# Performance work log

Measured on AMD Instinct MI355X. Metric: run time of the kernel, lower is better.

## Reference

```python
import jax, jax.numpy as jnp
import numpy as np
import math

B, L, D = 4, 4096, 768          # batch, seq_len (== l_max), d_model
ORDER, EMB_DIM = 16, 3          # hyena_filter_order, hyena_emb_dim
W_MOD = 1.0                     # hyena_w_mod
FAST, SLOW, TARGET = 0.3, 1.5, 1e-2  # ExponentialModulation defaults


def setup_inputs() -> dict:
    key = jax.random.key(0)
    ks = jax.random.split(key, 16)
    n = lambda i, shape, s: jax.random.normal(ks[i], shape, dtype=jnp.float32) * s
    # PositionalEmbedding buffer/param z, deterministic Hyena init (seq_len = l_max = L)
    t = np.linspace(0.0, 1.0, L)[None, :, None]
    bands = (EMB_DIM - 1) // 2
    t_re = np.linspace(0, L - 1, L)[None, :, None]
    w = 2 * math.pi * t_re / L
    f = np.linspace(1e-4, bands - 1, bands)[None, None]
    zc = np.exp(-1j * f * w)
    z = np.concatenate([t, zc.real, zc.imag], axis=-1).astype(np.float32)  # (1, L, 3)
    return {
        "u": jax.random.normal(ks[0], (B, L, D), dtype=jnp.float32),
        "w_in": n(1, (3 * D, D), 0.02),
        "b_in": jnp.zeros((3 * D,), jnp.float32),
        "w_out": n(2, (D, D), 0.02),
        "b_out": jnp.zeros((D,), jnp.float32),
        "conv_w": n(3, (3 * D, 1, 3), 0.3),   # depthwise Conv1d weight (O, I/groups=1, K)
        "conv_b": jnp.zeros((3 * D,), jnp.float32),
        "z": jnp.asarray(z),
        "fw1": n(4, (ORDER, EMB_DIM), 0.3),
        "fb1": n(5, (ORDER,), 0.3),
        "fw2": n(6, (ORDER, ORDER), 0.3),
        "fb2": n(7, (ORDER,), 0.3),
        "fw3": n(8, (ORDER, ORDER), 0.3),
        "fb3": n(9, (ORDER,), 0.3),
        "fw4": n(10, (D, ORDER), 0.3),
        "freq": jnp.full((1, ORDER), 10.0, jnp.float32),  # shared Sin freq, init w*ones
        "filter_bias": jax.random.normal(ks[11], (D,), dtype=jnp.float32),
    }


def _hyena_filter(z, fw1, fb1, fw2, fb2, fw3, fb3, fw4, freq, Lq):
    # implicit MLP with SHARED Sin activation (same freq param at all 3 activations)
    sin = lambda h: jnp.sin(W_MOD * freq * h)
    h = sin(z @ fw1.T + fb1)
    h = sin(h @ fw2.T + fb2)
    h = sin(h @ fw3.T + fb3)
    h = h @ fw4.T                                     # (1, L, D)
    # ExponentialModulation
    max_d = math.log(TARGET) / FAST
    min_d = math.log(TARGET) / SLOW
    deltas = jnp.linspace(min_d, max_d, D)[None, None]  # (1, 1, D)
    t = jnp.linspace(0.0, 1.0, Lq)[None, :, None]       # (1, L, 1)
    h = h * jnp.exp(-t * jnp.abs(deltas))
    return h[0].T                                      # (D, L)


def _fftconv(v, k, bias):
    # causal FFT long conv: fft_size = 2L, torch norm='forward' conventions
    Lq = v.shape[-1]
    nfft = 2 * Lq
    k_f = jnp.fft.rfft(k, n=nfft) / nfft               # (D, nfft//2+1)
    v_f = jnp.fft.rfft(v, n=nfft)                      # (B, D, nfft//2+1)
    y = jnp.fft.irfft(v_f * k_f, n=nfft, norm="forward")[..., :Lq]
    return y + v * bias[None, :, None]


def reference(u, w_in, b_in, w_out, b_out, conv_w, conv_b, z,
              fw1, fb1, fw2, fb2, fw3, fb3, fw4, freq, filter_bias):
    Bq, Lq, Dq = u.shape
    x = u @ w_in.T + b_in                              # (B, L, 3D)
    x = x.transpose(0, 2, 1)                           # (B, 3D, L)
    # depthwise short conv, kernel 3, padding 2, sliced to [:L]
    xc = jax.lax.conv_general_dilated(
        x, conv_w, window_strides=(1,), padding=[(2, 2)],
        feature_group_count=3 * Dq,
        dimension_numbers=("NCH", "OIH", "NCH"))[..., :Lq]
    xc = xc + conv_b[None, :, None]
    x1, x2, v = jnp.split(xc, 3, axis=1)               # each (B, D, L)
    v = v * x1                                         # pre-gate
    k = _hyena_filter(z[:, :Lq], fw1, fb1, fw2, fb2, fw3, fb3, fw4, freq, Lq)
    y = _fftconv(v, k, filter_bias) * x2               # long conv + post-gate
    y = y.transpose(0, 2, 1) @ w_out.T + b_out         # (B, L, D)
    return y
```

## Files before the change

kernel.cpp:

```cpp
#include <hip/hip_runtime.h>

#define BB 4
#define LL 4096
#define DD 768
#define TD 2304
#define NFFT 8192
#define PI2 6.283185307179586f

__device__ __forceinline__ unsigned short f2b(float f) {
    unsigned u = __float_as_uint(f);
    unsigned r = (u + 0x7fffu + ((u >> 16) & 1u)) >> 16;
    return (unsigned short)r;
}
__device__ __forceinline__ float b2f(unsigned short h) {
    return __uint_as_float((unsigned)h << 16);
}
__device__ __forceinline__ unsigned cvt_pk_bf16(float lo, float hi) {
    unsigned r;
    asm("v_cvt_pk_bf16_f32 %0, %1, %2" : "=v"(r) : "v"(lo), "v"(hi));
    return r;
}

typedef __bf16 bf16x8 __attribute__((ext_vector_type(8)));
typedef float  f32x4  __attribute__((ext_vector_type(4)));

constexpr float TWC[16] = {
    1.f, 0.98078528f, 0.92387953f, 0.83146961f,
    0.70710678f, 0.55557023f, 0.38268343f, 0.19509032f,
    0.f, -0.19509032f, -0.38268343f, -0.55557023f,
    -0.70710678f, -0.83146961f, -0.92387953f, -0.98078528f};
constexpr float TWS[16] = {
    0.f, 0.19509032f, 0.38268343f, 0.55557023f,
    0.70710678f, 0.83146961f, 0.92387953f, 0.98078528f,
    1.f, 0.98078528f, 0.92387953f, 0.83146961f,
    0.70710678f, 0.55557023f, 0.38268343f, 0.19509032f};

template<int LOGN, bool INV>
__device__ __forceinline__ void reg_fft(float2* R) {
    constexpr int N = 1 << LOGN;
#pragma unroll
    for (int i = 0; i < N; ++i) {
        int j = 0;
#pragma unroll
        for (int b = 0; b < LOGN; ++b) if (i & (1 << b)) j |= (1 << (LOGN - 1 - b));
        if (j > i) { float2 tt = R[i]; R[i] = R[j]; R[j] = tt; }
    }
#pragma unroll
    for (int s = 1; s <= LOGN; ++s) {
        const int hm = 1 << (s - 1);
        const int tsh = 5 - s;
#pragma unroll
        for (int g = 0; g < N; g += (hm << 1)) {
#pragma unroll
            for (int j2 = 0; j2 < hm; ++j2) {
                const float wr = TWC[j2 << tsh];
                const float wi = INV ? TWS[j2 << tsh] : -TWS[j2 << tsh];
                float2 u = R[g + j2];
                float2 v = R[g + j2 + hm];
                float vr = v.x * wr - v.y * wi;
                float vi = v.x * wi + v.y * wr;
                R[g + j2]      = make_float2(u.x + vr, u.y + vi);
                R[g + j2 + hm] = make_float2(u.x - vr, u.y - vi);
            }
        }
    }
}

template<int NN>
__device__ __forceinline__ void ramp_mul(float2* R, float ang) {
    float s0, c0; __sincosf(ang, &s0, &c0);
    float wr = c0, wi = s0;
#pragma unroll
    for (int k = 1; k < NN; ++k) {
        float xr = R[k].x, xi = R[k].y;
        R[k] = make_float2(xr * wr - xi * wi, xr * wi + xi * wr);
        float nr = wr * c0 - wi * s0;
        float ni = wr * s0 + wi * c0;
        wr = nr; wi = ni;
    }
}

#define A1(t, k2) ((k2) * 288 + (t) + ((t) >> 3))
#define A2(k2, p, r) ((k2) * 272 + (r) * 17 + (p))
#define FFT_LDS 9216

__device__ __forceinline__ void eng_fwd(float2* buf, float2* R, int t) {
    reg_fft<5, false>(R);
    ramp_mul<32>(R, -PI2 * (float)t / 8192.0f);
    __syncthreads();
#pragma unroll
    for (int k2 = 0; k2 < 32; ++k2) buf[A1(t, k2)] = R[k2];
    __syncthreads();
    const int p = t & 15, c2 = (t >> 4) << 1;
#pragma unroll
    for (int q = 0; q < 16; ++q) {
        R[q]      = buf[A1(p + 16 * q, c2)];
        R[16 + q] = buf[A1(p + 16 * q, c2 + 1)];
    }
    reg_fft<4, false>(R);
    reg_fft<4, false>(R + 16);
    float a2 = -PI2 * (float)p / 256.0f;
    ramp_mul<16>(R, a2);
    ramp_mul<16>(R + 16, a2);
    __syncthreads();
#pragma unroll
    for (int r = 0; r < 16; ++r) {
        buf[A2(c2, p, r)]     = R[r];
        buf[A2(c2 + 1, p, r)] = R[16 + r];
    }
    __syncthreads();
    const int rr = p;
#pragma unroll
    for (int pp = 0; pp < 16; ++pp) {
        R[pp]      = buf[A2(c2, pp, rr)];
        R[16 + pp] = buf[A2(c2 + 1, pp, rr)];
    }
    reg_fft<4, false>(R);
    reg_fft<4, false>(R + 16);
}

__device__ __forceinline__ void eng_inv(float2* buf, float2* R, int t) {
    const int p = t & 15, c2 = (t >> 4) << 1, rr = p;
    reg_fft<4, true>(R);
    reg_fft<4, true>(R + 16);
    __syncthreads();
#pragma unroll
    for (int pp = 0; pp < 16; ++pp) {
        buf[A2(c2, pp, rr)]     = R[pp];
        buf[A2(c2 + 1, pp, rr)] = R[16 + pp];
    }
    __syncthreads();
#pragma unroll
    for (int r = 0; r < 16; ++r) {
        R[r]      = buf[A2(c2, p, r)];
        R[16 + r] = buf[A2(c2 + 1, p, r)];
    }
    float a2 = PI2 * (float)p / 256.0f;
    ramp_mul<16>(R, a2);
    ramp_mul<16>(R + 16, a2);
    reg_fft<4, true>(R);
    reg_fft<4, true>(R + 16);
    __syncthreads();
#pragma unroll
    for (int q = 0; q < 16; ++q) {
        buf[A1(p + 16 * q, c2)]     = R[q];
        buf[A1(p + 16 * q, c2 + 1)] = R[16 + q];
    }
    __syncthreads();
#pragma unroll
    for (int k2 = 0; k2 < 32; ++k2) R[k2] = buf[A1(t, k2)];
    ramp_mul<32>(R, PI2 * (float)t / 8192.0f);
    reg_fft<5, true>(R);
}

__global__ __launch_bounds__(256) void k_cast_pair(
        const float* __restrict__ srcA, unsigned long long nA4,
        const float* __restrict__ srcB, unsigned long long nB4,
        unsigned short* __restrict__ dstA, unsigned short* __restrict__ dstB) {
    unsigned long long i = (unsigned long long)blockIdx.x * 256 + threadIdx.x;
    const float* s; unsigned short* d;
    if (i < nA4)            { s = srcA + i * 4;         d = dstA + i * 4; }
    else if (i < nA4 + nB4) { unsigned long long j = i - nA4; s = srcB + j * 4; d = dstB + j * 4; }
    else return;
    float4 v = *(const float4*)s;
    unsigned long long p = (unsigned long long)f2b(v.x)
                         | ((unsigned long long)f2b(v.y) << 16)
                         | ((unsigned long long)f2b(v.z) << 32)
                         | ((unsigned long long)f2b(v.w) << 48);
    *(unsigned long long*)d = p;
}

#define GEMM_CORE                                                               \
    __shared__ unsigned char AsB[16384];                                        \
    __shared__ unsigned char BsB[16384];                                        \
    const int tid  = threadIdx.x;                                               \
    const int lane = tid & 63;                                                  \
    const int w    = tid >> 6;                                                  \
    const int wr   = w >> 1, wc = w & 1;                                        \
    const int nbx  = (int)gridDim.x;                                            \
    int bid = (int)blockIdx.y * nbx + (int)blockIdx.x;                          \
    { const int cpx = (nbx * (int)gridDim.y) >> 3;                              \
      bid = (bid & 7) * cpx + (bid >> 3); }                                     \
    const int m0 = (bid / nbx) * 128, n0 = (bid % nbx) * 128;                   \
    f32x4 acc[4][4] = {};                                                       \
    const int srow = lane >> 3;                    \
    const int sslot = (lane & 7) ^ srow;          \
    for (int k0 = 0; k0 < K; k0 += 64) {                                        \
        _Pragma("unroll")                                                       \
        for (int c = 0; c < 4; ++c) {                                           \
            int chunk = w * 4 + c;                                              \
            int row = chunk * 8 + srow;                                         \
            const char* ga = (const char*)A  + (((size_t)(m0 + row) * K + k0) * 2) + sslot * 16; \
            __builtin_amdgcn_global_load_lds(                                   \
                (const __attribute__((address_space(1))) void*)ga,              \
                (__attribute__((address_space(3))) void*)(AsB + chunk * 1024), 16, 0, 0); \
            const char* gb = (const char*)Bw + (((size_t)(n0 + row) * K + k0) * 2) + sslot * 16; \
            __builtin_amdgcn_global_load_lds(                                   \
                (const __attribute__((address_space(1))) void*)gb,              \
                (__attribute__((address_space(3))) void*)(BsB + chunk * 1024), 16, 0, 0); \
        }                                                                       \
        __syncthreads();                                                        \
        const int quad = lane >> 4;                                             \
        const int rsel = lane & 15;                                             \
        _Pragma("unroll")                                                       \
        for (int kk = 0; kk < 2; ++kk) {                                        \
            bf16x8 af[4], bfr[4];                                               \
            _Pragma("unroll")                                                   \
            for (int i = 0; i < 4; ++i) {                                       \
                int rowA = wr * 64 + i * 16 + rsel;                             \
                int slotA = (kk * 4 + quad) ^ (rsel & 7);                       \
                af[i]  = *(const bf16x8*)(AsB + rowA * 128 + slotA * 16);       \
                int rowB = wc * 64 + i * 16 + rsel;                             \
                bfr[i] = *(const bf16x8*)(BsB + rowB * 128 + slotA * 16);       \
            }                                                                   \
            _Pragma("unroll")                                                   \
            for (int i = 0; i < 4; ++i)                                         \
                _Pragma("unroll")                                               \
                for (int j = 0; j < 4; ++j)                                     \
                    acc[i][j] = __builtin_amdgcn_mfma_f32_16x16x32_bf16(af[i], bfr[j], acc[i][j], 0, 0, 0); \
        }                                                                       \
        __syncthreads();                                                        \
    }

__global__ __launch_bounds__(256) void k_gemm1_xt(
        const unsigned short* __restrict__ A, const unsigned short* __restrict__ Bw,
        const float* __restrict__ bias, unsigned short* __restrict__ xT,
        int K) {
    GEMM_CORE
    const int cq = lane >> 4;
    const int cn = lane & 15;
    const int b  = m0 >> 12;
    const int lb = (m0 & 4095) + wr * 64 + cq * 4;
#pragma unroll
    for (int j = 0; j < 4; ++j) {
        int col = n0 + wc * 64 + j * 16 + cn;
        float bv = bias[col];
        unsigned short* cp = xT + ((size_t)b * TD + col) * LL + lb;
#pragma unroll
        for (int i = 0; i < 4; ++i) {
            uint2 p;
            p.x = cvt_pk_bf16(acc[i][j][0] + bv, acc[i][j][1] + bv);
            p.y = cvt_pk_bf16(acc[i][j][2] + bv, acc[i][j][3] + bv);
            *(uint2*)(cp + i * 16) = p;
        }
    }
}

__global__ __launch_bounds__(256) void k_gemm_mfma(
        const unsigned short* __restrict__ A, const unsigned short* __restrict__ Bw,
        const float* __restrict__ bias, float* __restrict__ C,
        int N, int K) {
    GEMM_CORE
    const int cq = lane >> 4;
    const int cn = lane & 15;
#pragma unroll
    for (int j = 0; j < 4; ++j) {
        int col = n0 + wc * 64 + j * 16 + cn;
        float bv = bias[col];
#pragma unroll
        for (int i = 0; i < 4; ++i) {
            int rbase = m0 + wr * 64 + i * 16 + cq * 4;
#pragma unroll
            for (int r = 0; r < 4; ++r)
                C[(size_t)(rbase + r) * N + col] = acc[i][j][r] + bv;
        }
    }
}

__device__ __forceinline__ void ld_row18(const unsigned short* __restrict__ r,
                                         int l0, float* a) {
    unsigned ql = 0;
    if (l0 >= 2) ql = *(const unsigned*)(r + l0 - 2);
    a[0] = b2f((unsigned short)(ql & 0xffffu));
    a[1] = b2f((unsigned short)(ql >> 16));
    uint4 q0 = *(const uint4*)(r + l0);
    uint4 q1 = *(const uint4*)(r + l0 + 8);
    unsigned qq[8] = {q0.x, q0.y, q0.z, q0.w, q1.x, q1.y, q1.z, q1.w};
#pragma unroll
    for (int k2 = 0; k2 < 8; ++k2) {
        a[2 + 2 * k2] = b2f((unsigned short)(qq[k2] & 0xffffu));
        a[3 + 2 * k2] = b2f((unsigned short)(qq[k2] >> 16));
    }
}

__global__ __launch_bounds__(256) void k_shortconv_t(
        const unsigned short* __restrict__ xT,
        const float* __restrict__ conv_w, const float* __restrict__ conv_b,
        unsigned short* __restrict__ vbuf, unsigned short* __restrict__ x2buf) {
    const int bd = blockIdx.x;
    const int b  = bd / DD;
    const int d  = bd - b * DD;
    const int l0 = (int)threadIdx.x << 4;
    const unsigned short* r1 = xT + ((size_t)b * TD + d) * LL;
    const unsigned short* r2 = r1 + (size_t)DD * LL;
    const unsigned short* r3 = r2 + (size_t)DD * LL;
    const float w10 = conv_w[3*d],          w11 = conv_w[3*d+1],          w12 = conv_w[3*d+2];
    const float w20 = conv_w[3*(DD+d)],     w21 = conv_w[3*(DD+d)+1],     w22 = conv_w[3*(DD+d)+2];
    const float w30 = conv_w[3*(2*DD+d)],   w31 = conv_w[3*(2*DD+d)+1],   w32 = conv_w[3*(2*DD+d)+2];
    const float c1 = conv_b[d], c2 = conv_b[DD + d], c3 = conv_b[2*DD + d];
    float a1[18], a2[18], a3[18];
    ld_row18(r1, l0, a1);
    ld_row18(r2, l0, a2);
    ld_row18(r3, l0, a3);
    unsigned pv[8], px[8];
#pragma unroll
    for (int k2 = 0; k2 < 8; ++k2) {
        float x1a = w10*a1[2*k2]   + w11*a1[2*k2+1] + w12*a1[2*k2+2] + c1;
        float x1b = w10*a1[2*k2+1] + w11*a1[2*k2+2] + w12*a1[2*k2+3] + c1;
        float x2a = w20*a2[2*k2]   + w21*a2[2*k2+1] + w22*a2[2*k2+2] + c2;
        float x2b = w20*a2[2*k2+1] + w21*a2[2*k2+2] + w22*a2[2*k2+3] + c2;
        float va  = w30*a3[2*k2]   + w31*a3[2*k2+1] + w32*a3[2*k2+2] + c3;
        float vb  = w30*a3[2*k2+1] + w31*a3[2*k2+2] + w32*a3[2*k2+3] + c3;
        pv[k2] = cvt_pk_bf16(va * x1a, vb * x1b);
        px[k2] = cvt_pk_bf16(x2a, x2b);
    }
    unsigned short* ov = vbuf  + ((size_t)b * DD + d) * LL + l0;
    unsigned short* ox = x2buf + ((size_t)b * DD + d) * LL + l0;
    *(uint4*)(ov)     = make_uint4(pv[0], pv[1], pv[2], pv[3]);
    *(uint4*)(ov + 8) = make_uint4(pv[4], pv[5], pv[6], pv[7]);
    *(uint4*)(ox)     = make_uint4(px[0], px[1], px[2], px[3]);
    *(uint4*)(ox + 8) = make_uint4(px[4], px[5], px[6], px[7]);
}

__global__ __launch_bounds__(256) void k_filter_mlp(
        const float* __restrict__ z,
        const float* __restrict__ fw1, const float* __restrict__ fb1,
        const float* __restrict__ fw2, const float* __restrict__ fb2,
        const float* __restrict__ fw3, const float* __restrict__ fb3,
        const float* __restrict__ freq, float* __restrict__ h3g) {
    int l = blockIdx.x * 256 + threadIdx.x;
    float z0 = z[l*3+0], z1 = z[l*3+1], z2 = z[l*3+2];
    float h1[16], h2[16];
#pragma unroll
    for (int j = 0; j < 16; ++j) {
        float a = z0*fw1[j*3+0] + z1*fw1[j*3+1] + z2*fw1[j*3+2] + fb1[j];
        h1[j] = sinf(freq[j] * a);
    }
#pragma unroll
    for (int j = 0; j < 16; ++j) {
        float a = fb2[j];
#pragma unroll
        for (int i = 0; i < 16; ++i) a += h1[i] * fw2[j*16+i];
        h2[j] = sinf(freq[j] * a);
    }
#pragma unroll
    for (int j = 0; j < 16; ++j) {
        float a = fb3[j];
#pragma unroll
        for (int i = 0; i < 16; ++i) a += h2[i] * fw3[j*16+i];
        h3g[j * LL + l] = sinf(freq[j] * a);
    }
}

__global__ __launch_bounds__(256) void k_filter_fft(
        const float* __restrict__ h3g, const float* __restrict__ fw4,
        const float* __restrict__ fbias, float2* __restrict__ kf) {
    __shared__ float2 buf[FFT_LDS];
    const int d = blockIdx.x, t = threadIdx.x;
    float w4[16];
#pragma unroll
    for (int i = 0; i < 16; ++i) w4[i] = fw4[d * 16 + i];
    const float min_d = 3.070113457325394f;
    const float max_d = 15.35056728662697f;
    const float ad = min_d + (max_d - min_d) * ((float)d / 767.0f);
    float2 R[32];
#pragma unroll
    for (int j = 0; j < 16; ++j) {
        int l = t + 256 * j;
        float acc = 0.f;
#pragma unroll
        for (int i = 0; i < 16; ++i) acc += h3g[i * LL + l] * w4[i];
        acc *= __expf(-((float)l / 4095.0f) * ad);
        R[j] = make_float2(acc, 0.f);
        R[16 + j] = make_float2(0.f, 0.f);
    }
    eng_fwd(buf, R, t);
    const float fb = fbias[d];
    const float inv_n = 1.0f / (float)NFFT;
    float2* kd = kf + (size_t)d * NFFT;
#pragma unroll
    for (int i = 0; i < 32; ++i)
        kd[i * 256 + t] = make_float2((R[i].x + fb) * inv_n, R[i].y * inv_n);
}

__global__ __launch_bounds__(256) void k_fftconv3(
        const unsigned short* __restrict__ vbuf, const float2* __restrict__ kf,
        unsigned short* __restrict__ x2y) {
    __shared__ float2 buf[FFT_LDS];
    const int bp = blockIdx.x;
    const int d = bp % DD;
    const int bpair = bp / DD;
    const size_t row1 = (size_t)(bpair * 2) * DD + d;
    const size_t row2 = row1 + DD;
    const unsigned short* v1 = vbuf + row1 * LL;
    const unsigned short* v2 = vbuf + row2 * LL;
    const int t = threadIdx.x;
    float2 R[32];
#pragma unroll
    for (int j = 0; j < 16; ++j) {
        int idx = t + 256 * j;
        R[j] = make_float2(b2f(v1[idx]), b2f(v2[idx]));
        R[16 + j] = make_float2(0.f, 0.f);
    }
    eng_fwd(buf, R, t);
    const float2* kd = kf + (size_t)d * NFFT;
#pragma unroll
    for (int i = 0; i < 32; ++i) {
        float2 w = kd[i * 256 + t];
        float2 zv = R[i];
        R[i] = make_float2(zv.x * w.x - zv.y * w.y, zv.x * w.y + zv.y * w.x);
    }
    eng_inv(buf, R, t);
    unsigned short* o1 = x2y + row1 * LL;
    unsigned short* o2 = x2y + row2 * LL;
#pragma unroll
    for (int j = 0; j < 16; ++j) {
        int idx = t + 256 * j;
        o1[idx] = f2b(R[j].x * b2f(o1[idx]));
        o2[idx] = f2b(R[j].y * b2f(o2[idx]));
    }
}

__global__ __launch_bounds__(256) void k_transpose_cast(
        const unsigned short* __restrict__ yg, unsigned short* __restrict__ ygT) {
    __shared__ float t[64][65];
    const int b = blockIdx.z;
    const int d0 = blockIdx.y * 64;
    const int l0 = blockIdx.x * 64;
    for (int idx = threadIdx.x; idx < 4096; idx += 256) {
        int r = idx >> 6, c = idx & 63;
        t[r][c] = b2f(yg[((size_t)(b * DD + d0 + r)) * LL + l0 + c]);
    }
    __syncthreads();
    for (int idx = threadIdx.x; idx < 2048; idx += 256) {
        int r = idx >> 5, c = (idx & 31) * 2;
        unsigned int p = (unsigned int)f2b(t[c][r]) | ((unsigned int)f2b(t[c+1][r]) << 16);
        *(unsigned int*)&ygT[((size_t)(b * LL + l0 + r)) * DD + d0 + c] = p;
    }
}

extern "C" void kernel_launch(void* const* d_in, const int* in_sizes, int n_in,
                              void* d_out, int out_size, void* d_ws, size_t ws_size,
                              hipStream_t stream) {
    const float* u      = (const float*)d_in[0];
    const float* w_in   = (const float*)d_in[1];
    const float* b_in   = (const float*)d_in[2];
    const float* w_out  = (const float*)d_in[3];
    const float* b_out  = (const float*)d_in[4];
    const float* conv_w = (const float*)d_in[5];
    const float* conv_b = (const float*)d_in[6];
    const float* z      = (const float*)d_in[7];
    const float* fw1    = (const float*)d_in[8];
    const float* fb1    = (const float*)d_in[9];
    const float* fw2    = (const float*)d_in[10];
    const float* fb2    = (const float*)d_in[11];
    const float* fw3    = (const float*)d_in[12];
    const float* fb3    = (const float*)d_in[13];
    const float* fw4    = (const float*)d_in[14];
    const float* freq   = (const float*)d_in[15];
    const float* fbias  = (const float*)d_in[16];

    char* ws = (char*)d_ws;
    unsigned short* x_bf     = (unsigned short*)(ws);
    float2* kf               = (float2*)(ws);
    float*  h3g              = (float*)(ws + 50331648);
    unsigned short* w_out_bf = (unsigned short*)(ws + 50593792);
    unsigned short* ygT      = (unsigned short*)(ws + 63176704);
    unsigned short* vbuf     = (unsigned short*)(ws + 150994944);
    unsigned short* x2y      = (unsigned short*)(ws + 176160768);
    unsigned short* u_bf     = (unsigned short*)(ws + 201326592);
    unsigned short* w_in_bf  = (unsigned short*)(ws + 226492416);

    k_cast_pair<<<(3145728 + 442368 + 255) / 256, 256, 0, stream>>>(
        u, 3145728ULL, w_in, 442368ULL, u_bf, w_in_bf);
    k_gemm1_xt<<<dim3(TD/128, (BB*LL)/128), 256, 0, stream>>>(u_bf, w_in_bf, b_in, x_bf, DD);
    k_shortconv_t<<<BB*DD, 256, 0, stream>>>(x_bf, conv_w, conv_b, vbuf, x2y);
    k_filter_mlp<<<LL/256, 256, 0, stream>>>(z, fw1, fb1, fw2, fb2, fw3, fb3, freq, h3g);
    k_filter_fft<<<DD, 256, 0, stream>>>(h3g, fw4, fbias, kf);
    k_cast_pair<<<(147456 + 255) / 256, 256, 0, stream>>>(
        w_out, 147456ULL, (const float*)0, 0ULL, w_out_bf, (unsigned short*)0);
    k_fftconv3<<<(BB/2)*DD, 256, 0, stream>>>(vbuf, kf, x2y);
    k_transpose_cast<<<dim3(LL/64, DD/64, BB), 256, 0, stream>>>(x2y, ygT);
    k_gemm_mfma<<<dim3(DD/128, (BB*LL)/128), 256, 0, stream>>>(ygT, w_out_bf, b_out, (float*)d_out, DD, DD);
}
```

Measured before the change: 410.3 us.

## Fuse depthwise short conv into FFT long-conv kernel, one block per channel

Folds the short convolution and pre-gate into the FFT convolution kernel. The conv output now goes through LDS into the FFT registers instead of being written as bf16 v and x2 buffers and read back. Each block handles one channel across all four batches (two batch pairs), so the filter spectrum is loaded once and reused. This removes a kernel launch and a global round trip of intermediates, but cuts the grid to 768 blocks, which lowers parallelism and occupancy. The workspace is laid out again so kf no longer aliases the GEMM output.

```diff
diff --git a/kernel.cpp b/kernel.cpp
--- a/kernel.cpp
+++ b/kernel.cpp
@@ -283,43 +283,82 @@
     }
 }
 
-__global__ __launch_bounds__(256) void k_shortconv_t(
+__global__ __launch_bounds__(256) void k_convfft(
         const unsigned short* __restrict__ xT,
         const float* __restrict__ conv_w, const float* __restrict__ conv_b,
-        unsigned short* __restrict__ vbuf, unsigned short* __restrict__ x2buf) {
-    const int bd = blockIdx.x;
-    const int b  = bd / DD;
-    const int d  = bd - b * DD;
-    const int l0 = (int)threadIdx.x << 4;
-    const unsigned short* r1 = xT + ((size_t)b * TD + d) * LL;
-    const unsigned short* r2 = r1 + (size_t)DD * LL;
-    const unsigned short* r3 = r2 + (size_t)DD * LL;
+        const float2* __restrict__ kf,
+        unsigned short* __restrict__ yg) {
+    __shared__ float2 buf[FFT_LDS];
+    const int d = blockIdx.x;
+    const int t = threadIdx.x;
+    const int l0 = t << 4;
     const float w10 = conv_w[3*d],          w11 = conv_w[3*d+1],          w12 = conv_w[3*d+2];
     const float w20 = conv_w[3*(DD+d)],     w21 = conv_w[3*(DD+d)+1],     w22 = conv_w[3*(DD+d)+2];
     const float w30 = conv_w[3*(2*DD+d)],   w31 = conv_w[3*(2*DD+d)+1],   w32 = conv_w[3*(2*DD+d)+2];
     const float c1 = conv_b[d], c2 = conv_b[DD + d], c3 = conv_b[2*DD + d];
-    float a1[18], a2[18], a3[18];
-    ld_row18(r1, l0, a1);
-    ld_row18(r2, l0, a2);
-    ld_row18(r3, l0, a3);
-    unsigned pv[8], px[8];
-#pragma unroll
-    for (int k2 = 0; k2 < 8; ++k2) {
-        float x1a = w10*a1[2*k2]   + w11*a1[2*k2+1] + w12*a1[2*k2+2] + c1;
-        float x1b = w10*a1[2*k2+1] + w11*a1[2*k2+2] + w12*a1[2*k2+3] + c1;
-        float x2a = w20*a2[2*k2]   + w21*a2[2*k2+1] + w22*a2[2*k2+2] + c2;
-        float x2b = w20*a2[2*k2+1] + w21*a2[2*k2+2] + w22*a2[2*k2+3] + c2;
-        float va  = w30*a3[2*k2]   + w31*a3[2*k2+1] + w32*a3[2*k2+2] + c3;
-        float vb  = w30*a3[2*k2+1] + w31*a3[2*k2+2] + w32*a3[2*k2+3] + c3;
-        pv[k2] = cvt_pk_bf16(va * x1a, vb * x1b);
-        px[k2] = cvt_pk_bf16(x2a, x2b);
-    }
-    unsigned short* ov = vbuf  + ((size_t)b * DD + d) * LL + l0;
-    unsigned short* ox = x2buf + ((size_t)b * DD + d) * LL + l0;
-    *(uint4*)(ov)     = make_uint4(pv[0], pv[1], pv[2], pv[3]);
-    *(uint4*)(ov + 8) = make_uint4(pv[4], pv[5], pv[6], pv[7]);
-    *(uint4*)(ox)     = make_uint4(px[0], px[1], px[2], px[3]);
-    *(uint4*)(ox + 8) = make_uint4(px[4], px[5], px[6], px[7]);
+    const float2* kd = kf + (size_t)d * NFFT;
+    float2 w[32];
+    float2*   vstage = buf;
+    unsigned* xstage = (unsigned*)(buf + 4096);
+
+#pragma unroll 1
+    for (int pair = 0; pair < 2; ++pair) {
+        const int b0 = pair * 2, b1 = b0 + 1;
+        {
+            float a[18], q1[16], vv0[16], vv1[16];
+            ld_row18(xT + ((size_t)b0 * TD + d) * LL, l0, a);
+#pragma unroll
+            for (int k = 0; k < 16; ++k) q1[k] = w10*a[k] + w11*a[k+1] + w12*a[k+2] + c1;
+            ld_row18(xT + ((size_t)b0 * TD + 2*DD + d) * LL, l0, a);
+#pragma unroll
+            for (int k = 0; k < 16; ++k) vv0[k] = (w30*a[k] + w31*a[k+1] + w32*a[k+2] + c3) * q1[k];
+            ld_row18(xT + ((size_t)b1 * TD + d) * LL, l0, a);
+#pragma unroll
+            for (int k = 0; k < 16; ++k) q1[k] = w10*a[k] + w11*a[k+1] + w12*a[k+2] + c1;
+            ld_row18(xT + ((size_t)b1 * TD + 2*DD + d) * LL, l0, a);
+#pragma unroll
+            for (int k = 0; k < 16; ++k) vv1[k] = (w30*a[k] + w31*a[k+1] + w32*a[k+2] + c3) * q1[k];
+#pragma unroll
+            for (int k = 0; k < 16; ++k) vstage[l0 + k] = make_float2(vv0[k], vv1[k]);
+            ld_row18(xT + ((size_t)b0 * TD + DD + d) * LL, l0, a);
+#pragma unroll
+            for (int k = 0; k < 16; ++k) q1[k] = w20*a[k] + w21*a[k+1] + w22*a[k+2] + c2;
+            ld_row18(xT + ((size_t)b1 * TD + DD + d) * LL, l0, a);
+#pragma unroll
+            for (int k = 0; k < 16; ++k)
+                xstage[l0 + k] = cvt_pk_bf16(q1[k], w20*a[k] + w21*a[k+1] + w22*a[k+2] + c2);
+        }
+        __syncthreads();
+        float2 R[32];
+        unsigned x2p[16];
+#pragma unroll
+        for (int j = 0; j < 16; ++j) {
+            int idx = t + 256 * j;
+            R[j] = vstage[idx];
+            x2p[j] = xstage[idx];
+            R[16 + j] = make_float2(0.f, 0.f);
+        }
+        if (pair == 0) {
+#pragma unroll
+            for (int i = 0; i < 32; ++i) w[i] = kd[i * 256 + t];
+        }
+        eng_fwd(buf, R, t);
+#pragma unroll
+        for (int i = 0; i < 32; ++i) {
+            float2 zv = R[i];
+            R[i] = make_float2(zv.x * w[i].x - zv.y * w[i].y, zv.x * w[i].y + zv.y * w[i].x);
+        }
+        eng_inv(buf, R, t);
+        unsigned short* o1 = yg + ((size_t)b0 * DD + d) * LL;
+        unsigned short* o2 = o1 + (size_t)DD * LL;
+#pragma unroll
+        for (int j = 0; j < 16; ++j) {
+            int idx = t + 256 * j;
+            o1[idx] = f2b(R[j].x * b2f((unsigned short)(x2p[j] & 0xffffu)));
+            o2[idx] = f2b(R[j].y * b2f((unsigned short)(x2p[j] >> 16)));
+        }
+        if (pair == 0) __syncthreads();
+    }
 }
 
 __global__ __launch_bounds__(256) void k_filter_mlp(
@@ -381,44 +420,6 @@
 #pragma unroll
     for (int i = 0; i < 32; ++i)
         kd[i * 256 + t] = make_float2((R[i].x + fb) * inv_n, R[i].y * inv_n);
-}
-
-__global__ __launch_bounds__(256) void k_fftconv3(
-        const unsigned short* __restrict__ vbuf, const float2* __restrict__ kf,
-        unsigned short* __restrict__ x2y) {
-    __shared__ float2 buf[FFT_LDS];
-    const int bp = blockIdx.x;
-    const int d = bp % DD;
-    const int bpair = bp / DD;
-    const size_t row1 = (size_t)(bpair * 2) * DD + d;
-    const size_t row2 = row1 + DD;
-    const unsigned short* v1 = vbuf + row1 * LL;
-    const unsigned short* v2 = vbuf + row2 * LL;
-    const int t = threadIdx.x;
-    float2 R[32];
-#pragma unroll
-    for (int j = 0; j < 16; ++j) {
-        int idx = t + 256 * j;
-        R[j] = make_float2(b2f(v1[idx]), b2f(v2[idx]));
-        R[16 + j] = make_float2(0.f, 0.f);
-    }
-    eng_fwd(buf, R, t);
-    const float2* kd = kf + (size_t)d * NFFT;
-#pragma unroll
-    for (int i = 0; i < 32; ++i) {
-        float2 w = kd[i * 256 + t];
-        float2 zv = R[i];
-        R[i] = make_float2(zv.x * w.x - zv.y * w.y, zv.x * w.y + zv.y * w.x);
-    }
-    eng_inv(buf, R, t);
-    unsigned short* o1 = x2y + row1 * LL;
-    unsigned short* o2 = x2y + row2 * LL;
-#pragma unroll
-    for (int j = 0; j < 16; ++j) {
-        int idx = t + 256 * j;
-        o1[idx] = f2b(R[j].x * b2f(o1[idx]));
-        o2[idx] = f2b(R[j].y * b2f(o2[idx]));
-    }
 }
 
 __global__ __launch_bounds__(256) void k_transpose_cast(
@@ -461,25 +462,23 @@
     const float* fbias  = (const float*)d_in[16];
 
     char* ws = (char*)d_ws;
-    unsigned short* x_bf     = (unsigned short*)(ws);
-    float2* kf               = (float2*)(ws);
-    float*  h3g              = (float*)(ws + 50331648);
-    unsigned short* w_out_bf = (unsigned short*)(ws + 50593792);
-    unsigned short* ygT      = (unsigned short*)(ws + 63176704);
-    unsigned short* vbuf     = (unsigned short*)(ws + 150994944);
-    unsigned short* x2y      = (unsigned short*)(ws + 176160768);
-    unsigned short* u_bf     = (unsigned short*)(ws + 201326592);
-    unsigned short* w_in_bf  = (unsigned short*)(ws + 226492416);
+    unsigned short* xT       = (unsigned short*)(ws);
+    float2* kf               = (float2*)(ws + 75497472);
+    float*  h3g              = (float*)(ws + 125829120);
+    unsigned short* w_out_bf = (unsigned short*)(ws + 126091264);
+    unsigned short* yg       = (unsigned short*)(ws + 127270912);
+    unsigned short* ygT      = (unsigned short*)(ws + 152436736);
+    unsigned short* u_bf     = (unsigned short*)(ws + 177602560);
+    unsigned short* w_in_bf  = (unsigned short*)(ws + 202768384);
 
     k_cast_pair<<<(3145728 + 442368 + 255) / 256, 256, 0, stream>>>(
         u, 3145728ULL, w_in, 442368ULL, u_bf, w_in_bf);
-    k_gemm1_xt<<<dim3(TD/128, (BB*LL)/128), 256, 0, stream>>>(u_bf, w_in_bf, b_in, x_bf, DD);
-    k_shortconv_t<<<BB*DD, 256, 0, stream>>>(x_bf, conv_w, conv_b, vbuf, x2y);
+    k_gemm1_xt<<<dim3(TD/128, (BB*LL)/128), 256, 0, stream>>>(u_bf, w_in_bf, b_in, xT, DD);
     k_filter_mlp<<<LL/256, 256, 0, stream>>>(z, fw1, fb1, fw2, fb2, fw3, fb3, freq, h3g);
     k_filter_fft<<<DD, 256, 0, stream>>>(h3g, fw4, fbias, kf);
     k_cast_pair<<<(147456 + 255) / 256, 256, 0, stream>>>(
         w_out, 147456ULL, (const float*)0, 0ULL, w_out_bf, (unsigned short*)0);
-    k_fftconv3<<<(BB/2)*DD, 256, 0, stream>>>(vbuf, kf, x2y);
-    k_transpose_cast<<<dim3(LL/64, DD/64, BB), 256, 0, stream>>>(x2y, ygT);
+    k_convfft<<<DD, 256, 0, stream>>>(xT, conv_w, conv_b, kf, yg);
+    k_transpose_cast<<<dim3(LL/64, DD/64, BB), 256, 0, stream>>>(yg, ygT);
     k_gemm_mfma<<<dim3(DD/128, (BB*LL)/128), 256, 0, stream>>>(ygT, w_out_bf, b_out, (float*)d_out, DD, DD);
 }
```

Result: slower. 550.3 us (+34.1%).
